# Performance work log

Hardware: AMD Instinct MI355X
Metric: run time of the kernel (lower is better)

## Reference

```python
import jax, jax.numpy as jnp
import numpy as np

# Le-ADMM constants (ADMM_Net init values; V_div_mat / R_div_mat are
# precomputed buffers in the torch code using these, not the learned mus)
MU1_0, MU2_0, MU3_0 = 1e-6, 1e-5, 4e-5
TAU_0 = 1e-4
ITERS = 5
BATCH = 8
SENSOR = (540, 960)


def _pad_full(v, sh):
    # zero-pad sensor-size (..., H, W) to full (..., 2H, 2W), centered
    H, W = sh
    pads = [(0, 0)] * (v.ndim - 2) + [(H // 2, H - H // 2), (W // 2, W - W // 2)]
    return jnp.pad(v, pads)


def _crop(v, sh):
    H, W = sh
    return v[..., H // 2:H // 2 + H, W // 2:W // 2 + W]


def _fft2(v):
    return jnp.fft.fft2(jnp.fft.ifftshift(v, axes=(-2, -1)), axes=(-2, -1))


def _ifft2(V):
    return jnp.fft.fftshift(jnp.fft.ifft2(V, axes=(-2, -1)), axes=(-2, -1))


def _Hop(x, Hf):
    return jnp.real(_ifft2(Hf * _fft2(x)))


def _Hadj(x, Hf):
    return jnp.real(_ifft2(jnp.conj(Hf) * _fft2(x)))


def _Psi(x):
    # forward finite differences (circular), vertical and horizontal
    return jnp.roll(x, 1, axis=-2) - x, jnp.roll(x, 1, axis=-1) - x


def _PsiT(uv, uh):
    return (jnp.roll(uv, -1, axis=-2) - uv) + (jnp.roll(uh, -1, axis=-1) - uh)


def _soft_iso(uv, uh, thresh):
    # isotropic soft-threshold on the 2D gradient magnitude
    mag = jnp.sqrt(uv * uv + uh * uh)
    mult = jnp.maximum(mag - thresh, 0.0) / jnp.maximum(mag, 1e-12)
    return uv * mult, uh * mult


def setup_inputs() -> dict:
    key = jax.random.key(0)
    k1, k2 = jax.random.split(key)
    x = jax.random.uniform(k1, (BATCH,) + SENSOR, dtype=jnp.float32)
    h = jax.random.uniform(k2, SENSOR, dtype=jnp.float32)
    h = h / jnp.linalg.norm(h)  # normalized PSF
    ones = jnp.ones((ITERS,), jnp.float32)
    return {
        "x": x,
        "h": h,
        "mu1": ones * MU1_0,
        "mu2": ones * MU2_0,
        "mu3": ones * MU3_0,
        "tau": ones * TAU_0,
    }


def reference(x, h, mu1, mu2, mu3, tau):
    sh = h.shape  # sensor size (H, W)
    fullH, fullW = 2 * sh[0], 2 * sh[1]

    Hf = _fft2(_pad_full(h[None], sh))[0]  # (2H, 2W) complex
    CtC = _pad_full(jnp.ones((1,) + sh, x.dtype), sh)[0]
    V_div = 1.0 / (CtC + MU1_0)
    lap = jnp.zeros((fullH, fullW), x.dtype)
    lap = (lap.at[0, 0].set(4.0).at[0, 1].set(-1.0).at[1, 0].set(-1.0)
           .at[0, -1].set(-1.0).at[-1, 0].set(-1.0))
    PsiTPsi = jnp.abs(jnp.fft.fft2(lap))
    R_div = 1.0 / (MU1_0 * jnp.abs(Hf) ** 2 + MU2_0 * PsiTPsi + MU3_0)

    Cty = _pad_full(x, sh)  # (B, 2H, 2W)
    zfull = jnp.zeros((x.shape[0], fullH, fullW), x.dtype)

    out = zfull
    for i in range(ITERS):
        # forward() calls admm.restValues() every iteration, so all ADMM state
        # (X, U, V, W, alphas) is zero at the start of each iteration: each
        # iteration is one ADMM step from zero state; output keeps the last.
        X, a1, a2v, a2h, a3 = zfull, zfull, zfull, zfull, zfull
        pv, ph = _Psi(X)
        Uv, Uh = _soft_iso(pv + a2v / mu2[i], ph + a2h / mu2[i], tau[i] / mu2[i])
        V = V_div * (a1 + mu1[i] * _Hop(X, Hf) + Cty)
        W = jnp.maximum(a3 / mu3[i] + X, 0.0)
        r = ((mu3[i] * W - a3)
             + _PsiT(mu2[i] * Uv - a2v, mu2[i] * Uh - a2h)
             + _Hadj(mu1[i] * V - a1, Hf))
        out = jnp.real(_ifft2(R_div * _fft2(r)))
    return _crop(out, sh)
```

## Files before the change

### kernel.cpp

```cpp
#include <hip/hip_runtime.h>


#define PI2 6.2831853071795864f

__device__ __forceinline__ float2 cadd(float2 a, float2 b){ return make_float2(a.x+b.x, a.y+b.y); }
__device__ __forceinline__ float2 csub(float2 a, float2 b){ return make_float2(a.x-b.x, a.y-b.y); }
__device__ __forceinline__ float2 cmul(float2 a, float2 b){ return make_float2(a.x*b.x - a.y*b.y, a.x*b.y + a.y*b.x); }
__device__ __forceinline__ float4 pk(float2 a, float2 b){ return make_float4(a.x,a.y,b.x,b.y); }

__device__ __forceinline__ int IDX(int a){ return a + (a >> 4); }
#define IDXSZ(n) ((n) + ((n) >> 4))
__device__ __forceinline__ int IDXP(int a){ return a + ((a >> 5) << 1); }
#define IDXPSZ(n) ((n) + (((n) >> 5) << 1) + 4)
__device__ __forceinline__ int IDX4(int a){ return a + (a >> 4); }
#define IDX4SZ(n) ((n) + ((n) >> 4) + 2)

__device__ __forceinline__ void ldp(const float2* __restrict__ b, int pos,
                                    float2& v0, float2& v1){
    const float4 t = *(const float4*)&b[IDXP(2*pos)];
    v0 = make_float2(t.x,t.y); v1 = make_float2(t.z,t.w);
}
__device__ __forceinline__ void stp(float2* __restrict__ b, int pos,
                                    float2 v0, float2 v1){
    *(float4*)&b[IDXP(2*pos)] = pk(v0, v1);
}
__device__ __forceinline__ void ld4(const float4* __restrict__ b, int pos,
                                    float2& v0, float2& v1){
    const float4 t = b[IDX4(pos)];
    v0 = make_float2(t.x,t.y); v1 = make_float2(t.z,t.w);
}
__device__ __forceinline__ void st4(float4* __restrict__ b, int pos,
                                    float2 v0, float2 v1){
    b[IDX4(pos)] = pk(v0, v1);
}

template<int DIR>
__device__ __forceinline__ void dft3(float2 x0, float2 x1, float2 x2,
                                     float2& y0, float2& y1, float2& y2)
{
    constexpr float s3 = (float)DIR * 0.8660254037844386f;
    float2 t = cadd(x1, x2), u = csub(x1, x2);
    float2 m = make_float2(x0.x - 0.5f*t.x, x0.y - 0.5f*t.y);
    float2 iu = make_float2(-s3*u.y, s3*u.x);
    y0 = cadd(x0, t); y1 = cadd(m, iu); y2 = csub(m, iu);
}

template<int DIR>
__device__ __forceinline__ void dft4(float2 a0, float2 a1, float2 a2, float2 a3,
                                     float2& b0, float2& b1, float2& b2, float2& b3)
{
    float2 t0 = cadd(a0,a2), t1 = csub(a0,a2), t2 = cadd(a1,a3), t3 = csub(a1,a3);
    float2 j3 = make_float2(-(float)DIR*t3.y, (float)DIR*t3.x);
    b0 = cadd(t0,t2); b2 = csub(t0,t2); b1 = cadd(t1,j3); b3 = csub(t1,j3);
}

template<int DIR>
__device__ __forceinline__ void dft6(const float2 a[6], float2 b[6])
{
    float2 e0,e1,e2,o0,o1,o2;
    dft3<DIR>(a[0],a[2],a[4], e0,e1,e2);
    dft3<DIR>(a[1],a[3],a[5], o0,o1,o2);
    constexpr float s3 = (float)DIR * 0.8660254037844386f;
    float2 w1 = make_float2( 0.5f, s3);
    float2 w2 = make_float2(-0.5f, s3);
    float2 t1 = cmul(w1,o1), t2 = cmul(w2,o2);
    b[0]=cadd(e0,o0); b[3]=csub(e0,o0);
    b[1]=cadd(e1,t1); b[4]=csub(e1,t1);
    b[2]=cadd(e2,t2); b[5]=csub(e2,t2);
}

template<int DIR>
__device__ __forceinline__ void dft8(const float2 a[8], float2 b[8])
{
    float2 e0,e1,e2,e3,o0,o1,o2,o3;
    dft4<DIR>(a[0],a[2],a[4],a[6], e0,e1,e2,e3);
    dft4<DIR>(a[1],a[3],a[5],a[7], o0,o1,o2,o3);
    constexpr float c = 0.70710678118654752f;
    float2 w1 = make_float2( c, (float)DIR*c);
    float2 w3 = make_float2(-c, (float)DIR*c);
    float2 t1 = cmul(w1,o1);
    float2 t2 = make_float2(-(float)DIR*o2.y, (float)DIR*o2.x);
    float2 t3 = cmul(w3,o3);
    b[0]=cadd(e0,o0); b[4]=csub(e0,o0);
    b[1]=cadd(e1,t1); b[5]=csub(e1,t1);
    b[2]=cadd(e2,t2); b[6]=csub(e2,t2);
    b[3]=cadd(e3,t3); b[7]=csub(e3,t3);
}

template<int DIR>
__device__ __forceinline__ void dft5(const float2 a[5], float2 b[5])
{
    constexpr float C1 = 0.30901699437494742f, S1c = 0.9510565162951535f;
    constexpr float C2 = -0.8090169943749475f, S2c = 0.5877852522924731f;
    float2 t1 = cadd(a[1],a[4]), t2 = cadd(a[2],a[3]), d1 = csub(a[1],a[4]), d2 = csub(a[2],a[3]);
    float2 m1 = make_float2(a[0].x + C1*t1.x + C2*t2.x, a[0].y + C1*t1.y + C2*t2.y);
    float2 m2 = make_float2(a[0].x + C2*t1.x + C1*t2.x, a[0].y + C2*t1.y + C1*t2.y);
    float2 e1 = make_float2(S1c*d1.x + S2c*d2.x, S1c*d1.y + S2c*d2.y);
    float2 e2 = make_float2(S2c*d1.x - S1c*d2.x, S2c*d1.y - S1c*d2.y);
    float2 ie1 = make_float2(-(float)DIR*e1.y, (float)DIR*e1.x);
    float2 ie2 = make_float2(-(float)DIR*e2.y, (float)DIR*e2.x);
    b[0] = make_float2(a[0].x + t1.x + t2.x, a[0].y + t1.y + t2.y);
    b[1] = cadd(m1, ie1); b[4] = csub(m1, ie1);
    b[2] = cadd(m2, ie2); b[3] = csub(m2, ie2);
}


__device__ __forceinline__ void row_s1_fwd_h(const float* __restrict__ xa,
                                             float2* __restrict__ bA, int tid)
{
    constexpr float STEP = -PI2 / 1920.0f;
    const float2 z = make_float2(0.f,0.f);
    for (int p = tid; p < 240; p += 256) {
        float2 a[8], b[8];
        a[0]=z; a[1]=z; a[6]=z; a[7]=z;
        a[2] = make_float2(xa[p],     0.f);
        a[3] = make_float2(xa[p+240], 0.f);
        a[4] = make_float2(xa[p+480], 0.f);
        a[5] = make_float2(xa[p+720], 0.f);
        dft8<-1>(a,b);
        float sv, cv; __sincosf(STEP * (float)p, &sv, &cv);
        float2 w1 = make_float2(cv, sv), w = w1;
        b[1] = cmul(b[1], w);
        #pragma unroll
        for (int u = 2; u < 8; ++u) { w = cmul(w, w1); b[u] = cmul(b[u], w); }
        #pragma unroll
        for (int u = 0; u < 8; ++u) bA[IDX(8*p + u)] = b[u];
    }
}

template<int DIR, int R, int NCUR, int S>
__device__ __forceinline__ void mid_stage(const float2* __restrict__ src,
                                          float2* __restrict__ dst, int tid)
{
    constexpr int M  = NCUR / R;
    constexpr int NB = M * S;
    constexpr float STEP = (float)DIR * PI2 / (float)NCUR;
    for (int i = tid; i < NB; i += 256) {
        const int p = i / S;
        float2 a[R], b[R];
        #pragma unroll
        for (int t = 0; t < R; ++t) a[t] = src[IDX(i + S*M*t)];
        if constexpr (R == 6) dft6<DIR>(a,b); else dft8<DIR>(a,b);
        float sv, cv; __sincosf(STEP * (float)p, &sv, &cv);
        float2 w1 = make_float2(cv, sv), w = w1;
        b[1] = cmul(b[1], w);
        #pragma unroll
        for (int u = 2; u < R; ++u) { w = cmul(w, w1); b[u] = cmul(b[u], w); }
        const int ob = (i - p*S) + S*(R*p);
        #pragma unroll
        for (int u = 0; u < R; ++u) dst[IDX(ob + S*u)] = b[u];
    }
}

__device__ __forceinline__ void row_fin5_store_h(const float2* __restrict__ src,
                                                 float2* __restrict__ gdst, int tid)
{
    for (int q = tid; q < 384; q += 256) {
        float2 a[5], b[5];
        #pragma unroll
        for (int u = 0; u < 5; ++u) a[u] = src[IDX(q + 384*u)];
        dft5<-1>(a,b);
        #pragma unroll
        for (int u = 0; u < 5; ++u) gdst[q + 384*u] = b[u];
    }
}


__device__ __forceinline__ void rp_s1_fwd(const float* __restrict__ xa,
                                          const float* __restrict__ xb,
                                          float4* __restrict__ sb, int tid)
{
    constexpr float STEP = -PI2 / 1920.0f;
    const float2 z = make_float2(0.f,0.f);
    for (int p = tid; p < 240; p += 256) {
        float2 a0[8], a1[8], b0[8], b1[8];
        a0[0]=a0[1]=a0[6]=a0[7]=z; a1[0]=a1[1]=a1[6]=a1[7]=z;
        #pragma unroll
        for (int t = 0; t < 4; ++t) {
            a0[2+t] = make_float2(xa[p+240*t],     xb[p+240*t]);
            a1[2+t] = make_float2(xa[960+p+240*t], xb[960+p+240*t]);
        }
        dft8<-1>(a0,b0); dft8<-1>(a1,b1);
        float sv, cv; __sincosf(STEP*(float)p, &sv, &cv);
        float2 w1 = make_float2(cv,sv), w = w1;
        b0[1]=cmul(b0[1],w); b1[1]=cmul(b1[1],w);
        #pragma unroll
        for (int u = 2; u < 8; ++u){ w = cmul(w,w1); b0[u]=cmul(b0[u],w); b1[u]=cmul(b1[u],w); }
        #pragma unroll
        for (int u = 0; u < 8; ++u) st4(sb, 8*p+u, b0[u], b1[u]);
    }
}

__device__ __forceinline__ void rp_s1_inv(const float2* __restrict__ Zr0,
                                          const float2* __restrict__ Zr1,
                                          float4* __restrict__ sb, int tid)
{
    constexpr float STEP = PI2 / 1920.0f;
    for (int p = tid; p < 240; p += 256) {
        float2 a0[8], a1[8], b0[8], b1[8];
        #pragma unroll
        for (int t = 0; t < 8; ++t) { a0[t] = Zr0[p+240*t]; a1[t] = Zr1[p+240*t]; }
        dft8<1>(a0,b0); dft8<1>(a1,b1);
        float sv, cv; __sincosf(STEP*(float)p, &sv, &cv);
        float2 w1 = make_float2(cv,sv), w = w1;
        b0[1]=cmul(b0[1],w); b1[1]=cmul(b1[1],w);
        #pragma unroll
        for (int u = 2; u < 8; ++u){ w = cmul(w,w1); b0[u]=cmul(b0[u],w); b1[u]=cmul(b1[u],w); }
        #pragma unroll
        for (int u = 0; u < 8; ++u) st4(sb, 8*p+u, b0[u], b1[u]);
    }
}

template<int DIR>
__device__ __forceinline__ void rp_mid8_ip(float4* __restrict__ sb, int tid)
{
    constexpr float STEP = (float)DIR * PI2 / 240.0f;
    const bool act = tid < 240;
    float2 b0[8], b1[8]; int ob = 0;
    if (act) {
        const int p = tid >> 3;
        float2 a0[8], a1[8];
        #pragma unroll
        for (int t = 0; t < 8; ++t) ld4(sb, tid + 240*t, a0[t], a1[t]);
        dft8<DIR>(a0,b0); dft8<DIR>(a1,b1);
        float sv, cv; __sincosf(STEP*(float)p, &sv, &cv);
        float2 w1 = make_float2(cv,sv), w = w1;
        b0[1]=cmul(b0[1],w); b1[1]=cmul(b1[1],w);
        #pragma unroll
        for (int u = 2; u < 8; ++u){ w = cmul(w,w1); b0[u]=cmul(b0[u],w); b1[u]=cmul(b1[u],w); }
        ob = (tid - 8*p) + 64*p;
    }
    __syncthreads();
    if (act) {
        #pragma unroll
        for (int u = 0; u < 8; ++u) st4(sb, ob + 8*u, b0[u], b1[u]);
    }
    __syncthreads();
}

template<int DIR>
__device__ __forceinline__ void rp_mid6_ip(float4* __restrict__ sb, int tid)
{
    constexpr float STEP = (float)DIR * PI2 / 30.0f;
    float2 c0[6], c1[6], d0[6], d1[6]; int ob0, ob1 = 0;
    {
        const int i = tid, p = i >> 6;
        float2 a0[6], a1[6];
        #pragma unroll
        for (int t = 0; t < 6; ++t) ld4(sb, i + 320*t, a0[t], a1[t]);
        dft6<DIR>(a0,c0); dft6<DIR>(a1,c1);
        float sv, cv; __sincosf(STEP*(float)p, &sv, &cv);
        float2 w1 = make_float2(cv,sv), w = w1;
        c0[1]=cmul(c0[1],w); c1[1]=cmul(c1[1],w);
        #pragma unroll
        for (int u = 2; u < 6; ++u){ w = cmul(w,w1); c0[u]=cmul(c0[u],w); c1[u]=cmul(c1[u],w); }
        ob0 = (i - 64*p) + 384*p;
    }
    const bool act2 = tid < 64;
    if (act2) {
        const int i = 256 + tid;
        float2 a0[6], a1[6];
        #pragma unroll
        for (int t = 0; t < 6; ++t) ld4(sb, i + 320*t, a0[t], a1[t]);
        dft6<DIR>(a0,d0); dft6<DIR>(a1,d1);
        float sv, cv; __sincosf(STEP*4.0f, &sv, &cv);
        float2 w1 = make_float2(cv,sv), w = w1;
        d0[1]=cmul(d0[1],w); d1[1]=cmul(d1[1],w);
        #pragma unroll
        for (int u = 2; u < 6; ++u){ w = cmul(w,w1); d0[u]=cmul(d0[u],w); d1[u]=cmul(d1[u],w); }
        ob1 = tid + 1536;
    }
    __syncthreads();
    {
        #pragma unroll
        for (int u = 0; u < 6; ++u) st4(sb, ob0 + 64*u, c0[u], c1[u]);
    }
    if (act2) {
        #pragma unroll
        for (int u = 0; u < 6; ++u) st4(sb, ob1 + 64*u, d0[u], d1[u]);
    }
    __syncthreads();
}

__device__ __forceinline__ void rp_fin5_storeZ(const float4* __restrict__ sb,
                                               float2* __restrict__ Zr0,
                                               float2* __restrict__ Zr1, int tid)
{
    for (int q = tid; q < 384; q += 256) {
        float2 a0[5],a1[5],b0[5],b1[5];
        #pragma unroll
        for (int u = 0; u < 5; ++u) ld4(sb, q + 384*u, a0[u], a1[u]);
        dft5<-1>(a0,b0); dft5<-1>(a1,b1);
        #pragma unroll
        for (int u = 0; u < 5; ++u) { Zr0[q+384*u] = b0[u]; Zr1[q+384*u] = b1[u]; }
    }
}

__device__ __forceinline__ void rp_fin5_crop(const float4* __restrict__ sb,
                                             float* __restrict__ oa0, float* __restrict__ ob0,
                                             float* __restrict__ oa1, float* __restrict__ ob1,
                                             int tid)
{
    for (int q = tid; q < 384; q += 256) {
        float2 a0[5],a1[5],b0[5],b1[5];
        #pragma unroll
        for (int u = 0; u < 5; ++u) ld4(sb, q + 384*u, a0[u], a1[u]);
        dft5<1>(a0,b0); dft5<1>(a1,b1);
        oa0[q+480] = b0[0].x; ob0[q+480] = b0[0].y;
        oa1[q+480] = b1[0].x; ob1[q+480] = b1[0].y;
        if (q < 96)   { oa0[q+864] = b0[1].x; ob0[q+864] = b0[1].y;
                        oa1[q+864] = b1[1].x; ob1[q+864] = b1[1].y; }
        if (q >= 288) { oa0[q-288] = b0[3].x; ob0[q-288] = b0[3].y;
                        oa1[q-288] = b1[3].x; ob1[q-288] = b1[3].y; }
        oa0[q+96]  = b0[4].x; ob0[q+96]  = b0[4].y;
        oa1[q+96]  = b1[4].x; ob1[q+96]  = b1[4].y;
    }
}


__device__ __forceinline__ void col_s1_fwd_pair(const float2* __restrict__ g, int c0,
                                                float2* __restrict__ bA, int tid)
{
    constexpr float STEP = -PI2 / 1080.0f;
    const float2 z = make_float2(0.f,0.f);
    const float4* gc = (const float4*)(g + c0);
    for (int p = tid; p < 180; p += 256) {
        float2 a0[6], a1[6], b0[6], b1[6];
        a0[0]=a0[5]=a1[0]=a1[5]=z;
        if (p >= 90) { float4 t = gc[(p-90)*960]; a0[1]=make_float2(t.x,t.y); a1[1]=make_float2(t.z,t.w); }
        else         { a0[1]=a1[1]=z; }
        { float4 t = gc[(p+90)*960];  a0[2]=make_float2(t.x,t.y); a1[2]=make_float2(t.z,t.w); }
        { float4 t = gc[(p+270)*960]; a0[3]=make_float2(t.x,t.y); a1[3]=make_float2(t.z,t.w); }
        if (p < 90)  { float4 t = gc[(p+450)*960]; a0[4]=make_float2(t.x,t.y); a1[4]=make_float2(t.z,t.w); }
        else         { a0[4]=a1[4]=z; }
        dft6<-1>(a0,b0); dft6<-1>(a1,b1);
        float sv, cv; __sincosf(STEP*(float)p, &sv, &cv);
        float2 w1 = make_float2(cv,sv), w = w1;
        b0[1]=cmul(b0[1],w); b1[1]=cmul(b1[1],w);
        #pragma unroll
        for (int u = 2; u < 6; ++u){ w = cmul(w,w1); b0[u]=cmul(b0[u],w); b1[u]=cmul(b1[u],w); }
        #pragma unroll
        for (int u = 0; u < 6; ++u) stp(bA, 6*p + u, b0[u], b1[u]);
    }
}

template<int DIR, int NCUR, int SC>
__device__ __forceinline__ void mid_pair(const float2* __restrict__ src,
                                         float2* __restrict__ dst, int tid)
{
    constexpr int NB = 180;
    constexpr float STEP = (float)DIR * PI2 / (float)NCUR;
    for (int ic = tid; ic < NB; ic += 256) {
        const int p = ic / SC;
        float2 a0[6], a1[6], b0[6], b1[6];
        #pragma unroll
        for (int t = 0; t < 6; ++t) ldp(src, ic + NB*t, a0[t], a1[t]);
        dft6<DIR>(a0,b0); dft6<DIR>(a1,b1);
        float sv, cv; __sincosf(STEP*(float)p, &sv, &cv);
        float2 w1 = make_float2(cv,sv), w = w1;
        b0[1]=cmul(b0[1],w); b1[1]=cmul(b1[1],w);
        #pragma unroll
        for (int u = 2; u < 6; ++u){ w = cmul(w,w1); b0[u]=cmul(b0[u],w); b1[u]=cmul(b1[u],w); }
        const int ob = (ic - p*SC) + SC*6*p;
        #pragma unroll
        for (int u = 0; u < 6; ++u) stp(dst, ob + SC*u, b0[u], b1[u]);
    }
}

template<int DIR, int NCUR, int SC>
__device__ __forceinline__ void mid_pair_ip(float2* __restrict__ buf, int tid)
{
    constexpr int NB = 180;
    constexpr float STEP = (float)DIR * PI2 / (float)NCUR;
    const bool act = tid < NB;
    float2 b0[6], b1[6]; int ob = 0;
    if (act) {
        const int p = tid / SC;
        float2 a0[6], a1[6];
        #pragma unroll
        for (int t = 0; t < 6; ++t) ldp(buf, tid + NB*t, a0[t], a1[t]);
        dft6<DIR>(a0,b0); dft6<DIR>(a1,b1);
        float sv, cv; __sincosf(STEP*(float)p, &sv, &cv);
        float2 w1 = make_float2(cv,sv), w = w1;
        b0[1]=cmul(b0[1],w); b1[1]=cmul(b1[1],w);
        #pragma unroll
        for (int u = 2; u < 6; ++u){ w = cmul(w,w1); b0[u]=cmul(b0[u],w); b1[u]=cmul(b1[u],w); }
        ob = (tid - p*SC) + SC*6*p;
    }
    __syncthreads();
    if (act) {
        #pragma unroll
        for (int u = 0; u < 6; ++u) stp(buf, ob + SC*u, b0[u], b1[u]);
    }
    __syncthreads();
}

__device__ __forceinline__ void fused5K5_ip(float2* __restrict__ buf,
                                            const float4* __restrict__ KI,
                                            int cpair, int tid)
{
    constexpr float STEP = PI2 / 1080.0f;
    const float4* Kc = KI + cpair*1080;
    const bool act = tid < 216;
    float2 d0[5], d1[5];
    if (act) {
        float2 a0[5],a1[5],s0[5],s1[5];
        #pragma unroll
        for (int u = 0; u < 5; ++u) ldp(buf, tid + 216*u, a0[u], a1[u]);
        dft5<-1>(a0,s0); dft5<-1>(a1,s1);
        #pragma unroll
        for (int u = 0; u < 5; ++u) {
            float4 kk = Kc[tid + 216*u];
            s0[u] = cmul(s0[u], make_float2(kk.x,kk.y));
            s1[u] = cmul(s1[u], make_float2(kk.z,kk.w));
        }
        dft5<1>(s0,d0); dft5<1>(s1,d1);
        float sv, cv; __sincosf(STEP*(float)tid, &sv, &cv);
        float2 w1 = make_float2(cv,sv), w = w1;
        d0[1]=cmul(d0[1],w); d1[1]=cmul(d1[1],w);
        #pragma unroll
        for (int u = 2; u < 5; ++u){ w = cmul(w,w1); d0[u]=cmul(d0[u],w); d1[u]=cmul(d1[u],w); }
    }
    __syncthreads();
    if (act) {
        #pragma unroll
        for (int u = 0; u < 5; ++u) stp(buf, 5*tid + u, d0[u], d1[u]);
    }
    __syncthreads();
}

__device__ __forceinline__ void fin6_crop_pair(const float2* __restrict__ src,
                                               float2* __restrict__ Zp,
                                               int c0, int tid)
{
    float4* gc = (float4*)(Zp + c0);
    for (int m = tid; m < 180; m += 256) {
        float2 a0[6],a1[6],b0[6],b1[6];
        #pragma unroll
        for (int t = 0; t < 6; ++t) ldp(src, m + 180*t, a0[t], a1[t]);
        dft6<1>(a0,b0); dft6<1>(a1,b1);
        gc[(m+270)*960] = pk(b0[0], b1[0]);
        if (m < 90)  gc[(m+450)*960] = pk(b0[1], b1[1]);
        if (m >= 90) gc[(m-90)*960]  = pk(b0[4], b1[4]);
        gc[(m+90)*960]  = pk(b0[5], b1[5]);
    }
}


__global__ __launch_bounds__(256,5) void k_row_fwd(const float* __restrict__ x,
                                                   const float* __restrict__ h,
                                                   float2* __restrict__ Z,
                                                   float2* __restrict__ Hrow)
{
    __shared__ float4 sb[IDX4SZ(1920)];
    const int tid = threadIdx.x;
    if (blockIdx.x < 1080) {
        const int pp = blockIdx.x / 270;
        const int r0 = (blockIdx.x % 270) * 2;
        const float* xa = x + ((2*pp  )*540 + r0)*960;
        const float* xb = x + ((2*pp+1)*540 + r0)*960;
        rp_s1_fwd(xa, xb, sb, tid); __syncthreads();
        rp_mid8_ip<-1>(sb, tid);
        rp_mid6_ip<-1>(sb, tid);
        float2* Zr0 = Z + (pp*540 + r0)*1920;
        rp_fin5_storeZ(sb, Zr0, Zr0 + 1920, tid);
    } else {
        float2* bA = (float2*)sb;
        float2* bB = bA + IDXSZ(1920);
        const int r = blockIdx.x - 1080;
        row_s1_fwd_h(h + r*960, bA, tid); __syncthreads();
        mid_stage<-1,8,240, 8>(bA, bB, tid); __syncthreads();
        mid_stage<-1,6, 30,64>(bB, bA, tid); __syncthreads();
        row_fin5_store_h(bA, Hrow + r*1920, tid);
    }
}

__global__ __launch_bounds__(256,4) void k_col_fft_h_buildK(const float2* __restrict__ Hrow,
                                                            const float* __restrict__ mu1,
                                                            float4* __restrict__ KI)
{
    __shared__ float2 bA[IDXPSZ(2160)], bB[IDXPSZ(2160)];
    const int tid = threadIdx.x;
    const int xcd = blockIdx.x & 7, idx = blockIdx.x >> 3;
    const int cpair = xcd*120 + idx, c0 = cpair*2;
    col_s1_fwd_pair(Hrow, c0, bA, tid);  __syncthreads();
    mid_pair<-1,180, 6>(bA, bB, tid);    __syncthreads();
    mid_pair<-1, 30,36>(bB, bA, tid);    __syncthreads();
    const float sc = mu1[4] / ((1.0f + 1e-6f) * 2073600.0f);
    const float cos0 = __cosf(PI2 * (float)(c0  ) * (1.0f/1920.0f));
    const float cos1 = __cosf(PI2 * (float)(c0+1) * (1.0f/1920.0f));
    float4* Kc = KI + cpair*1080;
    for (int p = tid; p < 216; p += 256) {
        float2 a0[5],a1[5],b0[5],b1[5];
        #pragma unroll
        for (int u = 0; u < 5; ++u) ldp(bA, p + 216*u, a0[u], a1[u]);
        dft5<-1>(a0,b0); dft5<-1>(a1,b1);
        #pragma unroll
        for (int u = 0; u < 5; ++u) {
            const int k = p + 216*u;
            const float cosk = __cosf(PI2 * (float)k * (1.0f/1080.0f));
            float m0 = b0[u].x*b0[u].x + b0[u].y*b0[u].y;
            float m1 = b1[u].x*b1[u].x + b1[u].y*b1[u].y;
            float f0 = sc / (1e-6f*m0 + 1e-5f*(4.0f - 2.0f*cosk - 2.0f*cos0) + 4e-5f);
            float f1 = sc / (1e-6f*m1 + 1e-5f*(4.0f - 2.0f*cosk - 2.0f*cos1) + 4e-5f);
            Kc[k] = make_float4(f0*b0[u].x, -f0*b0[u].y, f1*b1[u].x, -f1*b1[u].y);
        }
    }
}

__global__ __launch_bounds__(256,8) void k_col_fused(float2* __restrict__ Z,
                                                     const float4* __restrict__ KI)
{
    __shared__ float2 buf[IDXPSZ(2160)];
    const int tid = threadIdx.x;
    const int xcd = blockIdx.x & 7, idx = blockIdx.x >> 3;
    const int pp  = idx / 120;
    const int cpair = xcd*120 + (idx - pp*120), c0 = cpair*2;
    float2* Zp = Z + pp*540*1920;
    col_s1_fwd_pair(Zp, c0, buf, tid);  __syncthreads();
    mid_pair_ip<-1,180, 6>(buf, tid);
    mid_pair_ip<-1, 30,36>(buf, tid);
    fused5K5_ip(buf, KI, cpair, tid);
    mid_pair_ip< 1,216, 5>(buf, tid);
    mid_pair_ip< 1, 36,30>(buf, tid);
    fin6_crop_pair(buf, Zp, c0, tid);
}

__global__ __launch_bounds__(256,5) void k_row_inv_out(const float2* __restrict__ Z,
                                                       float* __restrict__ out)
{
    __shared__ float4 sb[IDX4SZ(1920)];
    const int tid = threadIdx.x;
    const int pp = blockIdx.x / 270;
    const int r0 = (blockIdx.x % 270) * 2;
    const float2* Zr0 = Z + (pp*540 + r0)*1920;
    rp_s1_inv(Zr0, Zr0 + 1920, sb, tid); __syncthreads();
    rp_mid8_ip<1>(sb, tid);
    rp_mid6_ip<1>(sb, tid);
    float* oa0 = out + ((2*pp  )*540 + r0)*960;
    float* ob0 = out + ((2*pp+1)*540 + r0)*960;
    rp_fin5_crop(sb, oa0, ob0, oa0 + 960, ob0 + 960, tid);
}

extern "C" void kernel_launch(void* const* d_in, const int* in_sizes, int n_in,
                              void* d_out, int out_size, void* d_ws, size_t ws_size,
                              hipStream_t stream)
{
    (void)in_sizes; (void)n_in; (void)out_size; (void)ws_size;
    const float* x   = (const float*)d_in[0];
    const float* h   = (const float*)d_in[1];
    const float* mu1 = (const float*)d_in[2];
    float*       out = (float*)d_out;

    float4* KI   = (float4*)d_ws;
    float2* Z    = (float2*)(KI + 960*1080);
    float2* Hrow = Z + 4*540*1920;

    k_row_fwd         <<<1620,   256, 0, stream>>>(x, h, Z, Hrow);
    k_col_fft_h_buildK<<<960,    256, 0, stream>>>(Hrow, mu1, KI);
    k_col_fused       <<<3840,   256, 0, stream>>>(Z, KI);
    k_row_inv_out     <<<1080,   256, 0, stream>>>(Z, out);
}
```

Before: 84.37 us.

## Process four columns per block with radix-10/12/9 column FFT stages

The column FFT kernel now handles four columns per block instead of two, and the 1080-point column transform is refactored from six radix stages (6,6,6,5 fused with K,5 inverse,6,6) into 10x12x9 factorizations (fwd10, mid12, fused 9-K-9, mid12 inverse, fin10). This cuts the number of shared-memory passes and block barriers and gives wider global accesses per row. In exchange, each thread holds more registers (launch bounds drop to 4 blocks per SM), the grid is halved, and some threads sit idle in stages that need only 216 or 240 lanes.

```diff
diff --git a/kernel.cpp b/kernel.cpp
--- a/kernel.cpp
+++ b/kernel.cpp
@@ -32,6 +32,15 @@
 __device__ __forceinline__ void st4(float4* __restrict__ b, int pos,
                                     float2 v0, float2 v1){
     b[IDX4(pos)] = pk(v0, v1);
+}
+__device__ __forceinline__ void ld4g(const float4* __restrict__ b, int pos, int g,
+                                     float2& v0, float2& v1){
+    const float4 t = b[IDX4(2*pos+g)];
+    v0 = make_float2(t.x,t.y); v1 = make_float2(t.z,t.w);
+}
+__device__ __forceinline__ void st4g(float4* __restrict__ b, int pos, int g,
+                                     float2 v0, float2 v1){
+    b[IDX4(2*pos+g)] = pk(v0, v1);
 }
 
 template<int DIR>
@@ -104,6 +113,62 @@
     b[2] = cadd(m2, ie2); b[3] = csub(m2, ie2);
 }
 
+template<int DIR>
+__device__ __forceinline__ void dft9(const float2 a[9], float2 b[9])
+{
+    float2 C0[3], C1[3], C2[3];
+    dft3<DIR>(a[0],a[3],a[6], C0[0],C0[1],C0[2]);
+    dft3<DIR>(a[1],a[4],a[7], C1[0],C1[1],C1[2]);
+    dft3<DIR>(a[2],a[5],a[8], C2[0],C2[1],C2[2]);
+    const float2 w91 = make_float2(0.7660444431189780f, (float)DIR*0.6427876096865393f);
+    const float2 w92 = make_float2(0.1736481776669304f, (float)DIR*0.9848077530122081f);
+    const float2 w94 = make_float2(-0.9396926207859084f, (float)DIR*0.3420201433256687f);
+    C1[1]=cmul(C1[1],w91); C1[2]=cmul(C1[2],w92);
+    C2[1]=cmul(C2[1],w92); C2[2]=cmul(C2[2],w94);
+    dft3<DIR>(C0[0],C1[0],C2[0], b[0],b[3],b[6]);
+    dft3<DIR>(C0[1],C1[1],C2[1], b[1],b[4],b[7]);
+    dft3<DIR>(C0[2],C1[2],C2[2], b[2],b[5],b[8]);
+}
+
+template<int DIR>
+__device__ __forceinline__ void dft10(const float2 a[10], float2 b[10])
+{
+    float2 ae[5] = {a[0],a[2],a[4],a[6],a[8]};
+    float2 ao[5] = {a[1],a[3],a[5],a[7],a[9]};
+    float2 E[5], O[5];
+    dft5<DIR>(ae, E); dft5<DIR>(ao, O);
+    const float2 w1 = make_float2( 0.8090169943749475f, (float)DIR*0.5877852522924731f);
+    const float2 w2 = make_float2( 0.3090169943749474f, (float)DIR*0.9510565162951535f);
+    const float2 w3 = make_float2(-0.3090169943749474f, (float)DIR*0.9510565162951535f);
+    const float2 w4 = make_float2(-0.8090169943749475f, (float)DIR*0.5877852522924731f);
+    float2 t1 = cmul(O[1],w1), t2 = cmul(O[2],w2), t3 = cmul(O[3],w3), t4 = cmul(O[4],w4);
+    b[0]=cadd(E[0],O[0]); b[5]=csub(E[0],O[0]);
+    b[1]=cadd(E[1],t1);   b[6]=csub(E[1],t1);
+    b[2]=cadd(E[2],t2);   b[7]=csub(E[2],t2);
+    b[3]=cadd(E[3],t3);   b[8]=csub(E[3],t3);
+    b[4]=cadd(E[4],t4);   b[9]=csub(E[4],t4);
+}
+
+template<int DIR>
+__device__ __forceinline__ void dft12(const float2 a[12], float2 b[12])
+{
+    float2 C0[4], C1[4], C2[4];
+    dft4<DIR>(a[0],a[3],a[6],a[9],  C0[0],C0[1],C0[2],C0[3]);
+    dft4<DIR>(a[1],a[4],a[7],a[10], C1[0],C1[1],C1[2],C1[3]);
+    dft4<DIR>(a[2],a[5],a[8],a[11], C2[0],C2[1],C2[2],C2[3]);
+    const float2 w121 = make_float2(0.8660254037844386f, (float)DIR*0.5f);
+    const float2 w122 = make_float2(0.5f, (float)DIR*0.8660254037844386f);
+    const float2 w124 = make_float2(-0.5f, (float)DIR*0.8660254037844386f);
+    C1[1]=cmul(C1[1],w121); C1[2]=cmul(C1[2],w122);
+    C1[3]=make_float2(-(float)DIR*C1[3].y, (float)DIR*C1[3].x);
+    C2[1]=cmul(C2[1],w122); C2[2]=cmul(C2[2],w124);
+    C2[3]=make_float2(-C2[3].x, -C2[3].y);
+    dft3<DIR>(C0[0],C1[0],C2[0], b[0],b[4],b[8]);
+    dft3<DIR>(C0[1],C1[1],C2[1], b[1],b[5],b[9]);
+    dft3<DIR>(C0[2],C1[2],C2[2], b[2],b[6],b[10]);
+    dft3<DIR>(C0[3],C1[3],C2[3], b[3],b[7],b[11]);
+}
+
 
 __device__ __forceinline__ void row_s1_fwd_h(const float* __restrict__ xa,
                                              float2* __restrict__ bA, int tid)
@@ -367,83 +432,121 @@
     }
 }
 
+
+__device__ __forceinline__ void c4_s1_fwd10(const float2* __restrict__ Zp, int c0,
+                                            float4* __restrict__ sb, int tid)
+{
+    constexpr float STEP = -PI2 / 1080.0f;
+    const float2 z = make_float2(0.f,0.f);
+    const float4* gc = (const float4*)(Zp + c0);
+    const bool act = tid < 216;
+    if (act) {
+        const int g = tid & 1, p = tid >> 1;
+        float2 a0[10], a1[10], b0[10], b1[10];
+        a0[0]=a0[1]=a0[8]=a0[9]=z; a1[0]=a1[1]=a1[8]=a1[9]=z;
+        if (p >= 54) { float4 t = gc[(p-54)*960+g]; a0[2]=make_float2(t.x,t.y); a1[2]=make_float2(t.z,t.w); }
+        else         { a0[2]=a1[2]=z; }
+        { float4 t = gc[(p+54)*960+g];  a0[3]=make_float2(t.x,t.y); a1[3]=make_float2(t.z,t.w); }
+        { float4 t = gc[(p+162)*960+g]; a0[4]=make_float2(t.x,t.y); a1[4]=make_float2(t.z,t.w); }
+        { float4 t = gc[(p+270)*960+g]; a0[5]=make_float2(t.x,t.y); a1[5]=make_float2(t.z,t.w); }
+        { float4 t = gc[(p+378)*960+g]; a0[6]=make_float2(t.x,t.y); a1[6]=make_float2(t.z,t.w); }
+        if (p < 54)  { float4 t = gc[(p+486)*960+g]; a0[7]=make_float2(t.x,t.y); a1[7]=make_float2(t.z,t.w); }
+        else         { a0[7]=a1[7]=z; }
+        dft10<-1>(a0,b0); dft10<-1>(a1,b1);
+        float sv, cv; __sincosf(STEP*(float)p, &sv, &cv);
+        float2 w1 = make_float2(cv,sv), w = w1;
+        b0[1]=cmul(b0[1],w); b1[1]=cmul(b1[1],w);
+        #pragma unroll
+        for (int u = 2; u < 10; ++u){ w = cmul(w,w1); b0[u]=cmul(b0[u],w); b1[u]=cmul(b1[u],w); }
+        #pragma unroll
+        for (int u = 0; u < 10; ++u) st4g(sb, 10*p+u, g, b0[u], b1[u]);
+    }
+    __syncthreads();
+}
+
 template<int DIR, int NCUR, int SC>
-__device__ __forceinline__ void mid_pair_ip(float2* __restrict__ buf, int tid)
-{
-    constexpr int NB = 180;
+__device__ __forceinline__ void c4_mid12_ip(float4* __restrict__ sb, int tid)
+{
+    constexpr int NB = (NCUR/12)*SC;
     constexpr float STEP = (float)DIR * PI2 / (float)NCUR;
-    const bool act = tid < NB;
-    float2 b0[6], b1[6]; int ob = 0;
+    const bool act = tid < 2*NB;
+    float2 b0[12], b1[12]; int ob = 0, g = 0;
     if (act) {
-        const int p = tid / SC;
-        float2 a0[6], a1[6];
-        #pragma unroll
-        for (int t = 0; t < 6; ++t) ldp(buf, tid + NB*t, a0[t], a1[t]);
-        dft6<DIR>(a0,b0); dft6<DIR>(a1,b1);
+        g = tid & 1;
+        const int ic = tid >> 1;
+        const int p = ic / SC;
+        float2 a0[12], a1[12];
+        #pragma unroll
+        for (int t = 0; t < 12; ++t) ld4g(sb, ic + NB*t, g, a0[t], a1[t]);
+        dft12<DIR>(a0,b0); dft12<DIR>(a1,b1);
         float sv, cv; __sincosf(STEP*(float)p, &sv, &cv);
         float2 w1 = make_float2(cv,sv), w = w1;
         b0[1]=cmul(b0[1],w); b1[1]=cmul(b1[1],w);
         #pragma unroll
-        for (int u = 2; u < 6; ++u){ w = cmul(w,w1); b0[u]=cmul(b0[u],w); b1[u]=cmul(b1[u],w); }
-        ob = (tid - p*SC) + SC*6*p;
+        for (int u = 2; u < 12; ++u){ w = cmul(w,w1); b0[u]=cmul(b0[u],w); b1[u]=cmul(b1[u],w); }
+        ob = (ic - p*SC) + SC*12*p;
     }
     __syncthreads();
     if (act) {
         #pragma unroll
-        for (int u = 0; u < 6; ++u) stp(buf, ob + SC*u, b0[u], b1[u]);
-    }
-    __syncthreads();
-}
-
-__device__ __forceinline__ void fused5K5_ip(float2* __restrict__ buf,
-                                            const float4* __restrict__ KI,
-                                            int cpair, int tid)
+        for (int u = 0; u < 12; ++u) st4g(sb, ob + SC*u, g, b0[u], b1[u]);
+    }
+    __syncthreads();
+}
+
+__device__ __forceinline__ void c4_f9K9_ip(float4* __restrict__ sb,
+                                           const float4* __restrict__ KI,
+                                           int cg, int tid)
 {
     constexpr float STEP = PI2 / 1080.0f;
-    const float4* Kc = KI + cpair*1080;
-    const bool act = tid < 216;
-    float2 d0[5], d1[5];
+    const bool act = tid < 240;
+    float2 d0[9], d1[9]; int q = 0, g = 0;
     if (act) {
-        float2 a0[5],a1[5],s0[5],s1[5];
-        #pragma unroll
-        for (int u = 0; u < 5; ++u) ldp(buf, tid + 216*u, a0[u], a1[u]);
-        dft5<-1>(a0,s0); dft5<-1>(a1,s1);
-        #pragma unroll
-        for (int u = 0; u < 5; ++u) {
-            float4 kk = Kc[tid + 216*u];
+        g = tid & 1; q = tid >> 1;
+        const float4* Kc = KI + (cg*2 + g)*1080;
+        float2 a0[9], a1[9], s0[9], s1[9];
+        #pragma unroll
+        for (int u = 0; u < 9; ++u) ld4g(sb, q + 120*u, g, a0[u], a1[u]);
+        dft9<-1>(a0,s0); dft9<-1>(a1,s1);
+        #pragma unroll
+        for (int u = 0; u < 9; ++u) {
+            float4 kk = Kc[q + 120*u];
             s0[u] = cmul(s0[u], make_float2(kk.x,kk.y));
             s1[u] = cmul(s1[u], make_float2(kk.z,kk.w));
         }
-        dft5<1>(s0,d0); dft5<1>(s1,d1);
-        float sv, cv; __sincosf(STEP*(float)tid, &sv, &cv);
+        dft9<1>(s0,d0); dft9<1>(s1,d1);
+        float sv, cv; __sincosf(STEP*(float)q, &sv, &cv);
         float2 w1 = make_float2(cv,sv), w = w1;
         d0[1]=cmul(d0[1],w); d1[1]=cmul(d1[1],w);
         #pragma unroll
-        for (int u = 2; u < 5; ++u){ w = cmul(w,w1); d0[u]=cmul(d0[u],w); d1[u]=cmul(d1[u],w); }
+        for (int u = 2; u < 9; ++u){ w = cmul(w,w1); d0[u]=cmul(d0[u],w); d1[u]=cmul(d1[u],w); }
     }
     __syncthreads();
     if (act) {
         #pragma unroll
-        for (int u = 0; u < 5; ++u) stp(buf, 5*tid + u, d0[u], d1[u]);
-    }
-    __syncthreads();
-}
-
-__device__ __forceinline__ void fin6_crop_pair(const float2* __restrict__ src,
-                                               float2* __restrict__ Zp,
-                                               int c0, int tid)
-{
+        for (int u = 0; u < 9; ++u) st4g(sb, 9*q + u, g, d0[u], d1[u]);
+    }
+    __syncthreads();
+}
+
+__device__ __forceinline__ void c4_fin10_crop(const float4* __restrict__ sb,
+                                              float2* __restrict__ Zp,
+                                              int c0, int tid)
+{
+    const bool act = tid < 216;
+    if (!act) return;
+    const int g = tid & 1, q = tid >> 1;
     float4* gc = (float4*)(Zp + c0);
-    for (int m = tid; m < 180; m += 256) {
-        float2 a0[6],a1[6],b0[6],b1[6];
-        #pragma unroll
-        for (int t = 0; t < 6; ++t) ldp(src, m + 180*t, a0[t], a1[t]);
-        dft6<1>(a0,b0); dft6<1>(a1,b1);
-        gc[(m+270)*960] = pk(b0[0], b1[0]);
-        if (m < 90)  gc[(m+450)*960] = pk(b0[1], b1[1]);
-        if (m >= 90) gc[(m-90)*960]  = pk(b0[4], b1[4]);
-        gc[(m+90)*960]  = pk(b0[5], b1[5]);
-    }
+    float2 a0[10], a1[10], b0[10], b1[10];
+    #pragma unroll
+    for (int u = 0; u < 10; ++u) ld4g(sb, q + 108*u, g, a0[u], a1[u]);
+    dft10<1>(a0,b0); dft10<1>(a1,b1);
+    gc[(q+270)*960+g] = pk(b0[0], b1[0]);
+    gc[(q+378)*960+g] = pk(b0[1], b1[1]);
+    if (q < 54)  gc[(q+486)*960+g] = pk(b0[2], b1[2]);
+    if (q >= 54) gc[(q-54)*960+g]  = pk(b0[7], b1[7]);
+    gc[(q+54)*960+g]  = pk(b0[8], b1[8]);
+    gc[(q+162)*960+g] = pk(b0[9], b1[9]);
 }
 
 
@@ -508,22 +611,21 @@
     }
 }
 
-__global__ __launch_bounds__(256,8) void k_col_fused(float2* __restrict__ Z,
+__global__ __launch_bounds__(256,4) void k_col_fused(float2* __restrict__ Z,
                                                      const float4* __restrict__ KI)
 {
-    __shared__ float2 buf[IDXPSZ(2160)];
+    __shared__ float4 sb[IDX4SZ(2160)];
     const int tid = threadIdx.x;
     const int xcd = blockIdx.x & 7, idx = blockIdx.x >> 3;
-    const int pp  = idx / 120;
-    const int cpair = xcd*120 + (idx - pp*120), c0 = cpair*2;
+    const int pp  = idx / 60;
+    const int cg  = xcd*60 + (idx - pp*60);
+    const int c0  = cg*4;
     float2* Zp = Z + pp*540*1920;
-    col_s1_fwd_pair(Zp, c0, buf, tid);  __syncthreads();
-    mid_pair_ip<-1,180, 6>(buf, tid);
-    mid_pair_ip<-1, 30,36>(buf, tid);
-    fused5K5_ip(buf, KI, cpair, tid);
-    mid_pair_ip< 1,216, 5>(buf, tid);
-    mid_pair_ip< 1, 36,30>(buf, tid);
-    fin6_crop_pair(buf, Zp, c0, tid);
+    c4_s1_fwd10(Zp, c0, sb, tid);
+    c4_mid12_ip<-1,108,10>(sb, tid);
+    c4_f9K9_ip(sb, KI, cg, tid);
+    c4_mid12_ip< 1,120, 9>(sb, tid);
+    c4_fin10_crop(sb, Zp, c0, tid);
 }
 
 __global__ __launch_bounds__(256,5) void k_row_inv_out(const float2* __restrict__ Z,
@@ -558,6 +660,6 @@
 
     k_row_fwd         <<<1620,   256, 0, stream>>>(x, h, Z, Hrow);
     k_col_fft_h_buildK<<<960,    256, 0, stream>>>(Hrow, mu1, KI);
-    k_col_fused       <<<3840,   256, 0, stream>>>(Z, KI);
+    k_col_fused       <<<1920,   256, 0, stream>>>(Z, KI);
     k_row_inv_out     <<<1080,   256, 0, stream>>>(Z, out);
 }
```

New measurement: 83.41 us. Within noise of the previous version (-1.1%).
